# Kernel optimization log

Hardware: AMD Instinct MI355X
Metric: run time of the kernel (lower is better)

Reference implementation:

```python
import jax, jax.numpy as jnp
import numpy as np

N, E, E_LBL = 50000, 800000, 200000
D_IN, H = 128, 128


def setup_inputs() -> dict:
    key = jax.random.key(0)
    ks = jax.random.split(key, 12)
    s = 0.05
    return {
        "x": jax.random.normal(ks[0], (N, D_IN), jnp.float32),
        "edge_index": jax.random.randint(ks[1], (2, E), 0, N, jnp.int64),
        "edge_label_index": jax.random.randint(ks[2], (2, E_LBL), 0, N, jnp.int64),
        "pre_w": jax.random.normal(ks[3], (D_IN, H), jnp.float32) * s,
        "pre_b": jax.random.normal(ks[4], (H,), jnp.float32) * s,
        "Wx": jax.random.normal(ks[5], (3, 2, H, H), jnp.float32) * s,  # gates z,r,h x cheb orders T0,T1
        "bx": jax.random.normal(ks[6], (3, H), jnp.float32) * s,
        "Wh": jax.random.normal(ks[7], (3, 2, H, H), jnp.float32) * s,
        "bh": jax.random.normal(ks[8], (3, H), jnp.float32) * s,
        "post_w": jax.random.normal(ks[9], (H, 2), jnp.float32) * s,
        "post_b": jax.random.normal(ks[10], (2,), jnp.float32) * s,
    }


def reference(x, edge_index, edge_label_index, pre_w, pre_b, Wx, bx, Wh, bh, post_w, post_b):
    n = x.shape[0]
    src, dst = edge_index[0], edge_index[1]

    # Scaled Chebyshev Laplacian (sym norm, lambda_max=2): L_hat = -D^{-1/2} A D^{-1/2}
    # (diagonal of L_hat is exactly 0, so only off-diagonal edge terms remain).
    deg = jax.ops.segment_sum(jnp.ones_like(src, dtype=x.dtype), src, num_segments=n)
    dinv = jnp.where(deg > 0, jax.lax.rsqrt(jnp.maximum(deg, 1.0)), 0.0)
    w = -(dinv[src] * dinv[dst])  # [E]

    def lap(v):  # L_hat @ v : gather src rows, weight, scatter-add at dst
        return jax.ops.segment_sum(w[:, None] * v[src], dst, num_segments=n)

    def cheb(v, Lv, W2, b):  # ChebConv K=2: T0(v)@W0 + T1(v)@W1 + b
        return v @ W2[0] + Lv @ W2[1] + b

    # pre: Linear(input_dim -> hidden)
    Xh = x @ pre_w + pre_b  # [N, H]
    LX = lap(Xh)

    # GConvGRU single step, H0 = 0
    Hc = jnp.zeros_like(Xh)
    LH = lap(Hc)
    Z = jax.nn.sigmoid(cheb(Xh, LX, Wx[0], bx[0]) + cheb(Hc, LH, Wh[0], bh[0]))
    R = jax.nn.sigmoid(cheb(Xh, LX, Wx[1], bx[1]) + cheb(Hc, LH, Wh[1], bh[1]))
    HR = Hc * R
    LHR = lap(HR)
    Ht = jnp.tanh(cheb(Xh, LX, Wx[2], bx[2]) + cheb(HR, LHR, Wh[2], bh[2]))
    Hc = Z * Hc + (1.0 - Z) * Ht

    h = jax.nn.relu(Hc)
    # link decoder: gather endpoints, hadamard, Linear(H->2), sum over logits
    hprod = h[edge_label_index[0]] * h[edge_label_index[1]]  # [E_lbl, H]
    out = hprod @ post_w + post_b  # [E_lbl, 2]
    return jnp.sum(out, axis=-1)  # [E_lbl]
```

## Files before the change

kernel.cpp:

```cpp
#include <hip/hip_runtime.h>
#include <math.h>


#define RND 2048
#define SORT_CAP 1536
#define CAPB 6144

typedef __attribute__((ext_vector_type(4))) float f32x4;
typedef __attribute__((ext_vector_type(8))) short short8;
typedef __attribute__((ext_vector_type(4))) unsigned u32x4;
typedef __attribute__((ext_vector_type(4))) int i32x4;

static __device__ __forceinline__ unsigned short f2b(float f) {
  union { float f; unsigned u; } v; v.f = f;
  unsigned r = (v.u + 0x7fffu + ((v.u >> 16) & 1u)) >> 16;
  return (unsigned short)r;
}
static __device__ __forceinline__ float b2f(unsigned short s) {
  union { unsigned u; float f; } v; v.u = ((unsigned)s) << 16;
  return v.f;
}

__global__ __launch_bounds__(256) void prep_kernel(const float* __restrict__ pre_w, const float* __restrict__ Wx,
                                                   const float* __restrict__ bx, const float* __restrict__ bh,
                                                   const float* __restrict__ post_w, const float* __restrict__ post_b,
                                                   unsigned short* __restrict__ Bt1c, unsigned short* __restrict__ Btc2,
                                                   float* __restrict__ fb2, float* __restrict__ pwsum,
                                                   int* __restrict__ binPos) {
  int e = blockIdx.x * 256 + threadIdx.x;
  if (e < 512) binPos[e * 16] = (e & 255) * CAPB;
  if (e < 16384) {
    int kc = e >> 12, r = e & 4095, col = r >> 5, kk = r & 31;
    Bt1c[e] = f2b(pre_w[(kc * 32 + kk) * 128 + col]);
  }
  int e2 = e - 16384;
  if (e2 >= 0 && e2 < 65536) {
    int kc = e2 >> 13, r = e2 & 8191, cB = r >> 5, kk = r & 31;
    int k = kc * 32 + kk, half = k >> 7, ki = k & 127;
    int cb = cB >> 7, r7 = cB & 127, nw6 = r7 >> 6, u2 = r7 & 63;
    int g = (u2 >= 32) ? 2 : 0, hcol = cb * 64 + nw6 * 32 + (u2 & 31);
    Btc2[e2] = f2b(Wx[((g * 2 + half) * 128 + ki) * 128 + hcol]);
  }
  int e3 = e - (16384 + 65536);
  if (e3 >= 0 && e3 < 256) {
    int cB = e3;
    int cb = cB >> 7, r7 = cB & 127, nw6 = r7 >> 6, u2 = r7 & 63;
    int g = (u2 >= 32) ? 2 : 0, hcol = cb * 64 + nw6 * 32 + (u2 & 31);
    fb2[cB] = bx[g * 128 + hcol] + bh[g * 128 + hcol];
  }
  int e4 = e - (16384 + 65536 + 256);
  if (e4 >= 0 && e4 < 128) pwsum[e4] = post_w[2 * e4] + post_w[2 * e4 + 1];
  if (e4 == 128) pwsum[128] = post_b[0] + post_b[1];
}

union SMemU {
  struct { unsigned short As[128 * 40]; unsigned short Bs[128 * 40]; } g;
  struct { unsigned ent[RND]; int hist[256], lstart[256], lofs[256], gbase[256], wsum[4];
           unsigned char ebin[RND], sb[RND]; } s;
};

__global__ __launch_bounds__(256) void mega1_kernel(const float* __restrict__ x,
                                                    const unsigned short* __restrict__ Bt1c,
                                                    const float* __restrict__ pre_b,
                                                    unsigned short* __restrict__ Xq,
                                                    const int* __restrict__ ei, int* __restrict__ binPos,
                                                    unsigned* __restrict__ bins,
                                                    unsigned char* __restrict__ sbins,
                                                    int N, int E, int RB) {
  __shared__ SMemU sm;
  const int t = threadIdx.x;

  if ((int)blockIdx.x < RB) {
    unsigned short* As = sm.g.As;
    unsigned short* Bs = sm.g.Bs;
    const int r0 = blockIdx.x * 128;
    const int w = t >> 6, lane = t & 63;
    const int m = lane & 15, q = lane >> 4;
    const int mw = (w >> 1) * 64, nw = (w & 1) * 64;

    f32x4 acc[4][4];
#pragma unroll
    for (int i = 0; i < 4; ++i)
#pragma unroll
      for (int j = 0; j < 4; ++j) acc[i][j] = {0.f, 0.f, 0.f, 0.f};

    const int arow = t >> 1, aseg = t & 1;
    const bool arow_ok = (r0 + arow) < N;
    const float* asrc0 = &x[(size_t)(r0 + arow) * 128 + aseg * 16];

    float4 cav[4]; short8 cbv0, cbv1;
    {
      if (arow_ok) {
#pragma unroll
        for (int i = 0; i < 4; ++i) cav[i] = *(const float4*)(asrc0 + i * 4);
      } else {
#pragma unroll
        for (int i = 0; i < 4; ++i) cav[i] = make_float4(0.f, 0.f, 0.f, 0.f);
      }
      const char* src = (const char*)Bt1c + t * 32;
      cbv0 = *(const short8*)src;
      cbv1 = *(const short8*)(src + 16);
    }

    for (int kc = 0; kc < 4; ++kc) {
      __syncthreads();
      {
        short8 t0, t1;
#pragma unroll
        for (int i = 0; i < 2; ++i) {
          t0[i * 4 + 0] = (short)f2b(cav[i].x); t0[i * 4 + 1] = (short)f2b(cav[i].y);
          t0[i * 4 + 2] = (short)f2b(cav[i].z); t0[i * 4 + 3] = (short)f2b(cav[i].w);
          t1[i * 4 + 0] = (short)f2b(cav[i + 2].x); t1[i * 4 + 1] = (short)f2b(cav[i + 2].y);
          t1[i * 4 + 2] = (short)f2b(cav[i + 2].z); t1[i * 4 + 3] = (short)f2b(cav[i + 2].w);
        }
        *(short8*)&As[arow * 40 + aseg * 16] = t0;
        *(short8*)&As[arow * 40 + aseg * 16 + 8] = t1;
        int bcol = t >> 1, boff = (t & 1) * 16;
        *(short8*)&Bs[bcol * 40 + boff] = cbv0;
        *(short8*)&Bs[bcol * 40 + boff + 8] = cbv1;
      }
      float4 nav[4]; short8 nbv0, nbv1;
      if (kc < 3) {
        if (arow_ok) {
          const float* src = asrc0 + (kc + 1) * 32;
#pragma unroll
          for (int i = 0; i < 4; ++i) nav[i] = *(const float4*)(src + i * 4);
        } else {
#pragma unroll
          for (int i = 0; i < 4; ++i) nav[i] = make_float4(0.f, 0.f, 0.f, 0.f);
        }
        const char* src = (const char*)Bt1c + (size_t)(kc + 1) * 8192 + t * 32;
        nbv0 = *(const short8*)src;
        nbv1 = *(const short8*)(src + 16);
      }
      __syncthreads();
      short8 af[4], bf[4];
#pragma unroll
      for (int i = 0; i < 4; ++i) af[i] = *(const short8*)&As[(mw + i * 16 + m) * 40 + q * 8];
#pragma unroll
      for (int j = 0; j < 4; ++j) bf[j] = *(const short8*)&Bs[(nw + j * 16 + m) * 40 + q * 8];
#pragma unroll
      for (int i = 0; i < 4; ++i)
#pragma unroll
        for (int j = 0; j < 4; ++j)
          acc[i][j] = __builtin_amdgcn_mfma_f32_16x16x32_bf16(af[i], bf[j], acc[i][j], 0, 0, 0);
      if (kc < 3) {
#pragma unroll
        for (int i = 0; i < 4; ++i) cav[i] = nav[i];
        cbv0 = nbv0; cbv1 = nbv1;
      }
    }

#pragma unroll
    for (int i = 0; i < 4; ++i) {
      int rb2 = r0 + mw + i * 16 + q * 4;
#pragma unroll
      for (int j = 0; j < 4; ++j) {
        int col = nw + j * 16 + m;
        float bias = pre_b[col];
#pragma unroll
        for (int r = 0; r < 4; ++r) {
          int row = rb2 + r;
          if (row < N) Xq[(size_t)row * 128 + col] = f2b(acc[i][j][r] + bias);
        }
      }
    }
    return;
  }

  unsigned* ent = sm.s.ent;
  unsigned char* ebin = sm.s.ebin;
  unsigned char* sb = sm.s.sb;
  int* hist = sm.s.hist;
  int* lstart = sm.s.lstart;
  int* lofs = sm.s.lofs;
  int* gbase = sm.s.gbase;
  int* wsum = sm.s.wsum;
  const int sbid = (int)blockIdx.x - RB;
  const int snum = (int)gridDim.x - RB;
  const int w = t >> 6, lane = t & 63;
  for (long long base = (long long)sbid * RND; base < E; base += (long long)snum * RND) {
    int cnt = (int)(((long long)E - base < RND) ? (E - base) : RND);
    if (t < 256) hist[t] = 0;
    __syncthreads();
    int my_s[8], my_d[8];
    {
      long long e0 = base + (long long)t * 8;
      if (e0 + 8 <= E && 8 * t + 8 <= cnt) {
        const i32x4* ps = (const i32x4*)&ei[e0];
        const i32x4* pd = (const i32x4*)&ei[E + e0];
        i32x4 s0 = ps[0], s1 = ps[1], d0 = pd[0], d1 = pd[1];
#pragma unroll
        for (int u = 0; u < 4; ++u) { my_s[u] = s0[u]; my_d[u] = d0[u]; }
#pragma unroll
        for (int u = 0; u < 4; ++u) { my_s[4 + u] = s1[u]; my_d[4 + u] = d1[u]; }
      } else {
#pragma unroll
        for (int u = 0; u < 8; ++u) {
          int i = t * 8 + u;
          my_s[u] = -1;
          if (i < cnt) { my_s[u] = ei[base + i]; my_d[u] = ei[E + base + i]; }
        }
      }
#pragma unroll
      for (int u = 0; u < 8; ++u)
        if (my_s[u] >= 0) atomicAdd(&hist[my_d[u] >> 8], 1);
    }
    __syncthreads();
    {
      int h = hist[t];
      hist[t] = 0;
      int v = h;
#pragma unroll
      for (int dd = 1; dd < 64; dd <<= 1) { int uu = __shfl_up(v, dd); if (lane >= dd) v += uu; }
      if (lane == 63) wsum[w] = v;
      __syncthreads();
      int woff = 0;
#pragma unroll
      for (int ww = 0; ww < 3; ++ww) if (ww < w) woff += wsum[ww];
      int excl = v - h + woff;
      lstart[t] = excl; lofs[t] = excl;
      if (h > 0) gbase[t] = atomicAdd(&binPos[t * 16], h);
    }
    __syncthreads();
#pragma unroll
    for (int u = 0; u < 8; ++u) {
      if (my_s[u] >= 0) {
        int b = my_d[u] >> 8;
        int p = atomicAdd(&lofs[b], 1);
        ent[p] = (unsigned)my_s[u] | ((unsigned)(my_d[u] & 255) << 16) | ((unsigned)b << 24);
        atomicAdd(&hist[my_s[u] >> 8], 1);
      }
    }
    __syncthreads();
    for (int i = t; i < cnt; i += 256) {
      unsigned e = ent[i];
      int b = e >> 24;
      int pos = gbase[b] + (i - lstart[b]);
      if (pos < (b + 1) * CAPB) bins[pos] = e;
    }
    __syncthreads();
    {
      int h = hist[t];
      int v = h;
#pragma unroll
      for (int dd = 1; dd < 64; dd <<= 1) { int uu = __shfl_up(v, dd); if (lane >= dd) v += uu; }
      if (lane == 63) wsum[w] = v;
      __syncthreads();
      int woff = 0;
#pragma unroll
      for (int ww = 0; ww < 3; ++ww) if (ww < w) woff += wsum[ww];
      int excl = v - h + woff;
      lstart[t] = excl; lofs[t] = excl;
      if (h > 0) gbase[t] = atomicAdd(&binPos[(256 + t) * 16], h);
    }
    __syncthreads();
#pragma unroll
    for (int u = 0; u < 8; ++u) {
      if (my_s[u] >= 0) {
        int b = my_s[u] >> 8;
        int p = atomicAdd(&lofs[b], 1);
        sb[p] = (unsigned char)(my_s[u] & 255);
        ebin[p] = (unsigned char)b;
      }
    }
    __syncthreads();
    for (int i = t; i < cnt; i += 256) {
      int b = ebin[i];
      int pos = gbase[b] + (i - lstart[b]);
      if (pos < (b + 1) * CAPB) sbins[pos] = sb[i];
    }
    __syncthreads();
  }
}

__global__ __launch_bounds__(256) void deghist_kernel(const unsigned char* __restrict__ sbins,
                                                      const int* __restrict__ binPos,
                                                      float* __restrict__ dinv, int N) {
  __shared__ int h[256];
  const int t = threadIdx.x;
  const int bin = blockIdx.x;
  h[t] = 0;
  __syncthreads();
  int T2 = binPos[(256 + bin) * 16] - bin * CAPB;
  if (T2 > CAPB) T2 = CAPB;
  const unsigned char* __restrict__ p = sbins + (size_t)bin * CAPB;
  for (int i = t; i < T2; i += 256) atomicAdd(&h[p[i]], 1);
  __syncthreads();
  int node = bin * 256 + t;
  if (node < N) dinv[node] = h[t] > 0 ? rsqrtf((float)h[t]) : 0.0f;
}

__global__ __launch_bounds__(512) void lap_bin_kernel(const unsigned short* __restrict__ Xq,
                                                      unsigned short* __restrict__ LXc,
                                                      const unsigned* __restrict__ bins,
                                                      const int* __restrict__ binPos,
                                                      const float* __restrict__ dinv, int N) {
  __shared__ unsigned eLDS[CAPB];
  __shared__ unsigned short sortS[SORT_CAP];
  __shared__ float sortW[SORT_CAP];
  __shared__ int hist[64], start[64], off[64];
  const int t = threadIdx.x;
  const int bin = blockIdx.x >> 2, qt = blockIdx.x & 3;
  const int lo = bin * CAPB;
  int T = binPos[bin * 16] - lo;
  if (T > CAPB) T = CAPB;
  const unsigned* __restrict__ ebase = &bins[lo];
  if (t < 64) hist[t] = 0;
  __syncthreads();
  for (int i = t; i < T; i += 512) {
    unsigned e = ebase[i];
    eLDS[i] = e;
    int dl = (e >> 16) & 255;
    if ((dl >> 6) == qt) atomicAdd(&hist[dl & 63], 1);
  }
  __syncthreads();
  if (t < 64) {
    int h = hist[t];
    int v = h;
#pragma unroll
    for (int d = 1; d < 64; d <<= 1) {
      int u = __shfl_up(v, d);
      if (t >= d) v += u;
    }
    start[t] = v - h;
    off[t] = v - h;
  }
  __syncthreads();
  for (int i = t; i < T; i += 512) {
    unsigned e = eLDS[i];
    int dl = (e >> 16) & 255;
    if ((dl >> 6) == qt) {
      int p = atomicAdd(&off[dl & 63], 1);
      if (p < SORT_CAP) {
        int s = (int)(e & 0xFFFFu);
        sortS[p] = (unsigned short)s;
        sortW[p] = dinv[s];
      }
    }
  }
  __syncthreads();
  const int wv = t >> 6, lane = t & 63;
  const int g4 = lane >> 4, sl = lane & 15;
  for (int n = wv; n < 64; n += 8) {
    int node = bin * 256 + qt * 64 + n;
    if (node >= N) break;
    int st = start[n], cnum = hist[n];
    float acc[8] = {0.f, 0.f, 0.f, 0.f, 0.f, 0.f, 0.f, 0.f};
    for (int j = 0; j < cnum; j += 8) {
#pragma unroll
      for (int u = 0; u < 2; ++u) {
        int idx = j + u * 4 + g4;
        bool val = idx < cnum;
        int si = st + (val ? idx : 0);
        int s = sortS[si];
        float ws = sortW[si];
        u32x4 vv = *(const u32x4*)((const char*)Xq + (size_t)s * 256 + sl * 16);
        if (val) {
#pragma unroll
          for (int k = 0; k < 4; ++k) {
            union { unsigned u32; float f; } fl, fh;
            fl.u32 = vv[k] << 16; fh.u32 = vv[k] & 0xffff0000u;
            acc[2 * k] += ws * fl.f;
            acc[2 * k + 1] += ws * fh.f;
          }
        }
      }
    }
#pragma unroll
    for (int k = 0; k < 8; ++k) {
      acc[k] += __shfl_xor(acc[k], 16);
      acc[k] += __shfl_xor(acc[k], 32);
    }
    if (g4 == 0) {
      float wd = -dinv[node];
      u32x4 o;
#pragma unroll
      for (int k = 0; k < 4; ++k)
        o[k] = (unsigned)f2b(acc[2 * k] * wd) | ((unsigned)f2b(acc[2 * k + 1] * wd) << 16);
      *(u32x4*)((char*)LXc + (size_t)node * 256 + sl * 16) = o;
    }
  }
}

__global__ __launch_bounds__(256) void gemm2_mfma(const unsigned short* __restrict__ Xq,
                                                  const unsigned short* __restrict__ LXc,
                                                  const unsigned short* __restrict__ Btc2,
                                                  const float* __restrict__ fb2,
                                                  unsigned short* __restrict__ hb, int N) {
  const int t = threadIdx.x;
  const int rb = blockIdx.x >> 1, cb = blockIdx.x & 1;
  const int r0 = rb * 128;
  const int w = t >> 6, lane = t & 63;
  const int m = lane & 15, q = lane >> 4;
  const int mw = (w >> 1) * 64, nw = (w & 1) * 64;

  f32x4 acc[4][4];
#pragma unroll
  for (int i = 0; i < 4; ++i)
#pragma unroll
    for (int j = 0; j < 4; ++j) acc[i][j] = {0.f, 0.f, 0.f, 0.f};

  size_t aoff[4];
#pragma unroll
  for (int i = 0; i < 4; ++i)
    aoff[i] = (size_t)(r0 + mw + i * 16 + m) * 256 + (size_t)q * 16;
  const char* bbase = (const char*)Btc2 + (size_t)(cb * 128 + nw + m) * 64 + (size_t)q * 16;

#pragma unroll 2
  for (int kc = 0; kc < 8; ++kc) {
    const char* abase = (kc < 4) ? (const char*)Xq : (const char*)LXc;
    const size_t ko = (size_t)(kc & 3) * 64;
    short8 af[4], bf[4];
#pragma unroll
    for (int i = 0; i < 4; ++i)
      af[i] = *(const short8*)(abase + aoff[i] + ko);
    const char* bk = bbase + (size_t)kc * 16384;
#pragma unroll
    for (int j = 0; j < 4; ++j)
      bf[j] = *(const short8*)(bk + (size_t)j * 16 * 64);
#pragma unroll
    for (int i = 0; i < 4; ++i)
#pragma unroll
      for (int j = 0; j < 4; ++j)
        acc[i][j] = __builtin_amdgcn_mfma_f32_16x16x32_bf16(af[i], bf[j], acc[i][j], 0, 0, 0);
  }

#pragma unroll
  for (int i = 0; i < 4; ++i) {
    int rbase = r0 + mw + i * 16 + q * 4;
#pragma unroll
    for (int jz = 0; jz < 2; ++jz) {
      int cBz = cb * 128 + nw + jz * 16 + m;
      int hc = cb * 64 + (nw >> 1) + jz * 16 + m;
      float bz = fb2[cBz], bt = fb2[cBz + 32];
#pragma unroll
      for (int r = 0; r < 4; ++r) {
        int row = rbase + r;
        if (row < N) {
          float zp = acc[i][jz][r] + bz;
          float tp = acc[i][jz + 2][r] + bt;
          float zs = 1.0f / (1.0f + __expf(-zp));
          float th = tanhf(tp);
          hb[(size_t)row * 128 + hc] = f2b(fmaxf((1.0f - zs) * th, 0.0f));
        }
      }
    }
  }
}

__global__ __launch_bounds__(256) void decoder_kernel(const unsigned short* __restrict__ hb,
                                                      const int* __restrict__ eli,
                                                      const float* __restrict__ pwsum, float* __restrict__ out, int M) {
  int t = threadIdx.x;
  int i = blockIdx.x * 16 + (t >> 4);
  int l = t & 15;
  if (i >= M) return;
  int a = eli[i], b = eli[M + i];
  int k = l * 8;
  short8 va = *(const short8*)&hb[(size_t)a * 128 + k];
  short8 vb = *(const short8*)&hb[(size_t)b * 128 + k];
  const float4* pwp = (const float4*)&pwsum[k];
  float4 p0 = pwp[0], p1 = pwp[1];
  float s = 0.0f;
  s += b2f((unsigned short)va[0]) * b2f((unsigned short)vb[0]) * p0.x;
  s += b2f((unsigned short)va[1]) * b2f((unsigned short)vb[1]) * p0.y;
  s += b2f((unsigned short)va[2]) * b2f((unsigned short)vb[2]) * p0.z;
  s += b2f((unsigned short)va[3]) * b2f((unsigned short)vb[3]) * p0.w;
  s += b2f((unsigned short)va[4]) * b2f((unsigned short)vb[4]) * p1.x;
  s += b2f((unsigned short)va[5]) * b2f((unsigned short)vb[5]) * p1.y;
  s += b2f((unsigned short)va[6]) * b2f((unsigned short)vb[6]) * p1.z;
  s += b2f((unsigned short)va[7]) * b2f((unsigned short)vb[7]) * p1.w;
#pragma unroll
  for (int off = 8; off; off >>= 1) s += __shfl_xor(s, off);
  if (l == 0) out[i] = s + pwsum[128];
}

extern "C" void kernel_launch(void* const* d_in, const int* in_sizes, int n_in,
                              void* d_out, int out_size, void* d_ws, size_t ws_size,
                              hipStream_t stream) {
  const float* x      = (const float*)d_in[0];
  const int*   ei     = (const int*)d_in[1];
  const int*   eli    = (const int*)d_in[2];
  const float* pre_w  = (const float*)d_in[3];
  const float* pre_b  = (const float*)d_in[4];
  const float* Wx     = (const float*)d_in[5];
  const float* bx     = (const float*)d_in[6];
  const float* bh     = (const float*)d_in[8];
  const float* post_w = (const float*)d_in[9];
  const float* post_b = (const float*)d_in[10];
  float* out = (float*)d_out;

  const int N = in_sizes[0] / 128;
  const int E = in_sizes[1] / 2;
  const int M = in_sizes[2] / 2;
  const int RB = (N + 127) / 128;
  const int NBIN = (N + 255) / 256;
  const int SCAT = (E + RND - 1) / RND;

  char* W = (char*)d_ws;
  size_t o = 0;
  float* dinv = (float*)(W + o); o += (size_t)N * 4;
  o = (o + 255) & ~(size_t)255;
  int* binPos = (int*)(W + o);    o += 512 * 16 * 4;
  o = (o + 255) & ~(size_t)255;
  unsigned* bins = (unsigned*)(W + o); o += (size_t)NBIN * CAPB * 4;
  o = (o + 255) & ~(size_t)255;
  unsigned char* sbins = (unsigned char*)(W + o); o += (size_t)NBIN * CAPB;
  o = (o + 255) & ~(size_t)255;
  unsigned short* Xq = (unsigned short*)(W + o);  o += (size_t)RB * 128 * 256;
  unsigned short* LXc = (unsigned short*)(W + o); o += (size_t)RB * 128 * 256;
  unsigned short* hb = (unsigned short*)(W + o);  o += (size_t)N * 256;
  unsigned short* Bt1c = (unsigned short*)(W + o); o += 32768;
  unsigned short* Btc2 = (unsigned short*)(W + o); o += 131072;
  float* fb2 = (float*)(W + o);  o += 1024;
  float* pwsum = (float*)(W + o); o += 768;

  prep_kernel<<<322, 256, 0, stream>>>(pre_w, Wx, bx, bh, post_w, post_b, Bt1c, Btc2, fb2, pwsum,
                                       binPos);
  mega1_kernel<<<RB + SCAT, 256, 0, stream>>>(x, Bt1c, pre_b, Xq, ei, binPos, bins, sbins, N, E, RB);
  deghist_kernel<<<NBIN, 256, 0, stream>>>(sbins, binPos, dinv, N);
  lap_bin_kernel<<<NBIN * 4, 512, 0, stream>>>(Xq, LXc, bins, binPos, dinv, N);
  gemm2_mfma<<<RB * 2, 256, 0, stream>>>(Xq, LXc, Btc2, fb2, hb, N);
  decoder_kernel<<<(M + 15) / 16, 256, 0, stream>>>(hb, eli, pwsum, out, M);
}
```

Baseline: 210.1 us.

## Split gemm2 across 8 waves and double-buffer fragment loads

The gemm2 MFMA kernel now runs 512 threads per block, giving each wave half the output columns (a z/tanh column pair) so per-wave accumulators shrink from 16 to 8 tiles. The k-loop is fully unrolled with ping-pong register buffers, so the next k-chunk's A/B fragments load while the current chunk's MFMAs run. The intent is to hide global load latency and raise occupancy through lower register pressure. The cost is that every A fragment is now loaded by twice as many waves.

```diff
diff --git a/kernel.cpp b/kernel.cpp
--- a/kernel.cpp
+++ b/kernel.cpp
@@ -383,7 +383,7 @@
   }
 }
 
-__global__ __launch_bounds__(256) void gemm2_mfma(const unsigned short* __restrict__ Xq,
+__global__ __launch_bounds__(512) void gemm2_mfma(const unsigned short* __restrict__ Xq,
                                                   const unsigned short* __restrict__ LXc,
                                                   const unsigned short* __restrict__ Btc2,
                                                   const float* __restrict__ fb2,
@@ -393,57 +393,78 @@
   const int r0 = rb * 128;
   const int w = t >> 6, lane = t & 63;
   const int m = lane & 15, q = lane >> 4;
-  const int mw = (w >> 1) * 64, nw = (w & 1) * 64;
-
-  f32x4 acc[4][4];
-#pragma unroll
-  for (int i = 0; i < 4; ++i)
-#pragma unroll
-    for (int j = 0; j < 4; ++j) acc[i][j] = {0.f, 0.f, 0.f, 0.f};
+  const int mw = (w >> 2) * 64;
+  const int wc = w & 3;
+  const int nw64 = (wc >> 1) * 64, jo = wc & 1;
+  const int cZ = cb * 128 + nw64 + jo * 16 + m;
+
+  f32x4 acc[4][2];
+#pragma unroll
+  for (int i = 0; i < 4; ++i) { acc[i][0] = {0.f,0.f,0.f,0.f}; acc[i][1] = {0.f,0.f,0.f,0.f}; }
 
   size_t aoff[4];
 #pragma unroll
   for (int i = 0; i < 4; ++i)
     aoff[i] = (size_t)(r0 + mw + i * 16 + m) * 256 + (size_t)q * 16;
-  const char* bbase = (const char*)Btc2 + (size_t)(cb * 128 + nw + m) * 64 + (size_t)q * 16;
-
-#pragma unroll 2
+  const char* bbase = (const char*)Btc2 + (size_t)cZ * 64 + (size_t)q * 16;
+
+  short8 afA[4], bfA[2], afB[4], bfB[2];
+  {
+    const char* ab = (const char*)Xq;
+#pragma unroll
+    for (int i = 0; i < 4; ++i) afA[i] = *(const short8*)(ab + aoff[i]);
+    bfA[0] = *(const short8*)(bbase);
+    bfA[1] = *(const short8*)(bbase + 32 * 64);
+  }
+#pragma unroll
   for (int kc = 0; kc < 8; ++kc) {
-    const char* abase = (kc < 4) ? (const char*)Xq : (const char*)LXc;
-    const size_t ko = (size_t)(kc & 3) * 64;
-    short8 af[4], bf[4];
-#pragma unroll
-    for (int i = 0; i < 4; ++i)
-      af[i] = *(const short8*)(abase + aoff[i] + ko);
-    const char* bk = bbase + (size_t)kc * 16384;
-#pragma unroll
-    for (int j = 0; j < 4; ++j)
-      bf[j] = *(const short8*)(bk + (size_t)j * 16 * 64);
-#pragma unroll
-    for (int i = 0; i < 4; ++i)
-#pragma unroll
-      for (int j = 0; j < 4; ++j)
-        acc[i][j] = __builtin_amdgcn_mfma_f32_16x16x32_bf16(af[i], bf[j], acc[i][j], 0, 0, 0);
-  }
-
+    const bool even = (kc & 1) == 0;
+    if (kc < 7) {
+      const int kn = kc + 1;
+      const char* ab = (kn < 4) ? (const char*)Xq : (const char*)LXc;
+      const size_t ko = (size_t)(kn & 3) * 64;
+      const char* bk = bbase + (size_t)kn * 16384;
+      if (even) {
+#pragma unroll
+        for (int i = 0; i < 4; ++i) afB[i] = *(const short8*)(ab + aoff[i] + ko);
+        bfB[0] = *(const short8*)(bk);
+        bfB[1] = *(const short8*)(bk + 32 * 64);
+      } else {
+#pragma unroll
+        for (int i = 0; i < 4; ++i) afA[i] = *(const short8*)(ab + aoff[i] + ko);
+        bfA[0] = *(const short8*)(bk);
+        bfA[1] = *(const short8*)(bk + 32 * 64);
+      }
+    }
+    if (even) {
+#pragma unroll
+      for (int i = 0; i < 4; ++i) {
+        acc[i][0] = __builtin_amdgcn_mfma_f32_16x16x32_bf16(afA[i], bfA[0], acc[i][0], 0, 0, 0);
+        acc[i][1] = __builtin_amdgcn_mfma_f32_16x16x32_bf16(afA[i], bfA[1], acc[i][1], 0, 0, 0);
+      }
+    } else {
+#pragma unroll
+      for (int i = 0; i < 4; ++i) {
+        acc[i][0] = __builtin_amdgcn_mfma_f32_16x16x32_bf16(afB[i], bfB[0], acc[i][0], 0, 0, 0);
+        acc[i][1] = __builtin_amdgcn_mfma_f32_16x16x32_bf16(afB[i], bfB[1], acc[i][1], 0, 0, 0);
+      }
+    }
+  }
+
+  const float bz = fb2[cZ], bt = fb2[cZ + 32];
+  const int hc = cb * 64 + (nw64 >> 1) + jo * 16 + m;
 #pragma unroll
   for (int i = 0; i < 4; ++i) {
     int rbase = r0 + mw + i * 16 + q * 4;
 #pragma unroll
-    for (int jz = 0; jz < 2; ++jz) {
-      int cBz = cb * 128 + nw + jz * 16 + m;
-      int hc = cb * 64 + (nw >> 1) + jz * 16 + m;
-      float bz = fb2[cBz], bt = fb2[cBz + 32];
-#pragma unroll
-      for (int r = 0; r < 4; ++r) {
-        int row = rbase + r;
-        if (row < N) {
-          float zp = acc[i][jz][r] + bz;
-          float tp = acc[i][jz + 2][r] + bt;
-          float zs = 1.0f / (1.0f + __expf(-zp));
-          float th = tanhf(tp);
-          hb[(size_t)row * 128 + hc] = f2b(fmaxf((1.0f - zs) * th, 0.0f));
-        }
+    for (int r = 0; r < 4; ++r) {
+      int row = rbase + r;
+      if (row < N) {
+        float zp = acc[i][0][r] + bz;
+        float tp = acc[i][1][r] + bt;
+        float zs = 1.0f / (1.0f + __expf(-zp));
+        float th = tanhf(tp);
+        hb[(size_t)row * 128 + hc] = f2b(fmaxf((1.0f - zs) * th, 0.0f));
       }
     }
   }
@@ -521,6 +542,6 @@
   mega1_kernel<<<RB + SCAT, 256, 0, stream>>>(x, Bt1c, pre_b, Xq, ei, binPos, bins, sbins, N, E, RB);
   deghist_kernel<<<NBIN, 256, 0, stream>>>(sbins, binPos, dinv, N);
   lap_bin_kernel<<<NBIN * 4, 512, 0, stream>>>(Xq, LXc, bins, binPos, dinv, N);
-  gemm2_mfma<<<RB * 2, 256, 0, stream>>>(Xq, LXc, Btc2, fb2, hb, N);
+  gemm2_mfma<<<RB * 2, 512, 0, stream>>>(Xq, LXc, Btc2, fb2, hb, N);
   decoder_kernel<<<(M + 15) / 16, 256, 0, stream>>>(hb, eli, pwsum, out, M);
 }
```

Measured after the change: 216.6 us. +3.1%, slower.

## Fuse Laplacian aggregation with gate GEMM, keep LX tile in LDS

Applied to the files above, without the earlier changes.

Merges the binned Laplacian kernel and the MFMA gate GEMM into one kernel. Each 64-node block writes its bf16 L·X rows into LDS (reusing the edge staging buffer through a union) and then runs the second GEMM directly, reading Xq from global and LX from LDS. This removes the LX round trip through global memory and one kernel launch. In exchange each block computes a 64x256 output tile with 8 waves, which gives less B-matrix reuse than the old 128-row tiles, and the GEMM now waits behind the gather phase in every block.

```diff
diff --git a/kernel.cpp b/kernel.cpp
--- a/kernel.cpp
+++ b/kernel.cpp
@@ -291,12 +291,17 @@
   if (node < N) dinv[node] = h[t] > 0 ? rsqrtf((float)h[t]) : 0.0f;
 }
 
-__global__ __launch_bounds__(512) void lap_bin_kernel(const unsigned short* __restrict__ Xq,
-                                                      unsigned short* __restrict__ LXc,
-                                                      const unsigned* __restrict__ bins,
-                                                      const int* __restrict__ binPos,
-                                                      const float* __restrict__ dinv, int N) {
-  __shared__ unsigned eLDS[CAPB];
+__global__ __launch_bounds__(512) void lap_gemm2_kernel(const unsigned short* __restrict__ Xq,
+                                                        const unsigned* __restrict__ bins,
+                                                        const int* __restrict__ binPos,
+                                                        const float* __restrict__ dinv,
+                                                        const unsigned short* __restrict__ Btc2,
+                                                        const float* __restrict__ fb2,
+                                                        unsigned short* __restrict__ hb, int N) {
+  __shared__ union {
+    unsigned eLDS[CAPB];
+    unsigned short lx[64 * 136];
+  } u;
   __shared__ unsigned short sortS[SORT_CAP];
   __shared__ float sortW[SORT_CAP];
   __shared__ int hist[64], start[64], off[64];
@@ -310,7 +315,7 @@
   __syncthreads();
   for (int i = t; i < T; i += 512) {
     unsigned e = ebase[i];
-    eLDS[i] = e;
+    u.eLDS[i] = e;
     int dl = (e >> 16) & 255;
     if ((dl >> 6) == qt) atomicAdd(&hist[dl & 63], 1);
   }
@@ -320,15 +325,15 @@
     int v = h;
 #pragma unroll
     for (int d = 1; d < 64; d <<= 1) {
-      int u = __shfl_up(v, d);
-      if (t >= d) v += u;
+      int uu = __shfl_up(v, d);
+      if (t >= d) v += uu;
     }
     start[t] = v - h;
     off[t] = v - h;
   }
   __syncthreads();
   for (int i = t; i < T; i += 512) {
-    unsigned e = eLDS[i];
+    unsigned e = u.eLDS[i];
     int dl = (e >> 16) & 255;
     if ((dl >> 6) == qt) {
       int p = atomicAdd(&off[dl & 63], 1);
@@ -349,8 +354,8 @@
     float acc[8] = {0.f, 0.f, 0.f, 0.f, 0.f, 0.f, 0.f, 0.f};
     for (int j = 0; j < cnum; j += 8) {
 #pragma unroll
-      for (int u = 0; u < 2; ++u) {
-        int idx = j + u * 4 + g4;
+      for (int uu = 0; uu < 2; ++uu) {
+        int idx = j + uu * 4 + g4;
         bool val = idx < cnum;
         int si = st + (val ? idx : 0);
         int s = sortS[si];
@@ -378,57 +383,58 @@
 #pragma unroll
       for (int k = 0; k < 4; ++k)
         o[k] = (unsigned)f2b(acc[2 * k] * wd) | ((unsigned)f2b(acc[2 * k + 1] * wd) << 16);
-      *(u32x4*)((char*)LXc + (size_t)node * 256 + sl * 16) = o;
-    }
-  }
-}
-
-__global__ __launch_bounds__(256) void gemm2_mfma(const unsigned short* __restrict__ Xq,
-                                                  const unsigned short* __restrict__ LXc,
-                                                  const unsigned short* __restrict__ Btc2,
-                                                  const float* __restrict__ fb2,
-                                                  unsigned short* __restrict__ hb, int N) {
-  const int t = threadIdx.x;
-  const int rb = blockIdx.x >> 1, cb = blockIdx.x & 1;
-  const int r0 = rb * 128;
-  const int w = t >> 6, lane = t & 63;
+      *(u32x4*)((char*)u.lx + (size_t)n * 272 + sl * 16) = o;
+    }
+  }
+  __syncthreads();
+
   const int m = lane & 15, q = lane >> 4;
-  const int mw = (w >> 1) * 64, nw = (w & 1) * 64;
-
-  f32x4 acc[4][4];
-#pragma unroll
-  for (int i = 0; i < 4; ++i)
-#pragma unroll
-    for (int j = 0; j < 4; ++j) acc[i][j] = {0.f, 0.f, 0.f, 0.f};
-
-  size_t aoff[4];
-#pragma unroll
-  for (int i = 0; i < 4; ++i)
-    aoff[i] = (size_t)(r0 + mw + i * 16 + m) * 256 + (size_t)q * 16;
+  const int mwl = (wv >> 2) * 32;
+  const int wc = wv & 3;
+  const int cb = wc >> 1, nw = (wc & 1) * 64;
+  const int r0 = bin * 256 + qt * 64;
+
+  f32x4 acc2[2][4];
+#pragma unroll
+  for (int i = 0; i < 2; ++i)
+#pragma unroll
+    for (int j = 0; j < 4; ++j) acc2[i][j] = {0.f, 0.f, 0.f, 0.f};
+
+  size_t aoff[2];
+#pragma unroll
+  for (int i = 0; i < 2; ++i) {
+    int ar = r0 + mwl + i * 16 + m;
+    if (ar >= N) ar = 0;
+    aoff[i] = (size_t)ar * 256 + (size_t)q * 16;
+  }
   const char* bbase = (const char*)Btc2 + (size_t)(cb * 128 + nw + m) * 64 + (size_t)q * 16;
 
-#pragma unroll 2
+#pragma unroll
   for (int kc = 0; kc < 8; ++kc) {
-    const char* abase = (kc < 4) ? (const char*)Xq : (const char*)LXc;
-    const size_t ko = (size_t)(kc & 3) * 64;
-    short8 af[4], bf[4];
-#pragma unroll
-    for (int i = 0; i < 4; ++i)
-      af[i] = *(const short8*)(abase + aoff[i] + ko);
+    short8 af[2], bf[4];
+    if (kc < 4) {
+#pragma unroll
+      for (int i = 0; i < 2; ++i)
+        af[i] = *(const short8*)((const char*)Xq + aoff[i] + (size_t)kc * 64);
+    } else {
+#pragma unroll
+      for (int i = 0; i < 2; ++i)
+        af[i] = *(const short8*)((const char*)u.lx + (size_t)(mwl + i * 16 + m) * 272 + (size_t)q * 16 + (size_t)(kc - 4) * 64);
+    }
     const char* bk = bbase + (size_t)kc * 16384;
 #pragma unroll
     for (int j = 0; j < 4; ++j)
-      bf[j] = *(const short8*)(bk + (size_t)j * 16 * 64);
-#pragma unroll
-    for (int i = 0; i < 4; ++i)
+      bf[j] = *(const short8*)(bk + (size_t)j * 1024);
+#pragma unroll
+    for (int i = 0; i < 2; ++i)
 #pragma unroll
       for (int j = 0; j < 4; ++j)
-        acc[i][j] = __builtin_amdgcn_mfma_f32_16x16x32_bf16(af[i], bf[j], acc[i][j], 0, 0, 0);
-  }
-
-#pragma unroll
-  for (int i = 0; i < 4; ++i) {
-    int rbase = r0 + mw + i * 16 + q * 4;
+        acc2[i][j] = __builtin_amdgcn_mfma_f32_16x16x32_bf16(af[i], bf[j], acc2[i][j], 0, 0, 0);
+  }
+
+#pragma unroll
+  for (int i = 0; i < 2; ++i) {
+    int rbase = r0 + mwl + i * 16 + q * 4;
 #pragma unroll
     for (int jz = 0; jz < 2; ++jz) {
       int cBz = cb * 128 + nw + jz * 16 + m;
@@ -438,8 +444,8 @@
       for (int r = 0; r < 4; ++r) {
         int row = rbase + r;
         if (row < N) {
-          float zp = acc[i][jz][r] + bz;
-          float tp = acc[i][jz + 2][r] + bt;
+          float zp = acc2[i][jz][r] + bz;
+          float tp = acc2[i][jz + 2][r] + bt;
           float zs = 1.0f / (1.0f + __expf(-zp));
           float th = tanhf(tp);
           hb[(size_t)row * 128 + hc] = f2b(fmaxf((1.0f - zs) * th, 0.0f));
@@ -509,7 +515,6 @@
   unsigned char* sbins = (unsigned char*)(W + o); o += (size_t)NBIN * CAPB;
   o = (o + 255) & ~(size_t)255;
   unsigned short* Xq = (unsigned short*)(W + o);  o += (size_t)RB * 128 * 256;
-  unsigned short* LXc = (unsigned short*)(W + o); o += (size_t)RB * 128 * 256;
   unsigned short* hb = (unsigned short*)(W + o);  o += (size_t)N * 256;
   unsigned short* Bt1c = (unsigned short*)(W + o); o += 32768;
   unsigned short* Btc2 = (unsigned short*)(W + o); o += 131072;
@@ -520,7 +525,6 @@
                                        binPos);
   mega1_kernel<<<RB + SCAT, 256, 0, stream>>>(x, Bt1c, pre_b, Xq, ei, binPos, bins, sbins, N, E, RB);
   deghist_kernel<<<NBIN, 256, 0, stream>>>(sbins, binPos, dinv, N);
-  lap_bin_kernel<<<NBIN * 4, 512, 0, stream>>>(Xq, LXc, bins, binPos, dinv, N);
-  gemm2_mfma<<<RB * 2, 256, 0, stream>>>(Xq, LXc, Btc2, fb2, hb, N);
+  lap_gemm2_kernel<<<NBIN * 4, 512, 0, stream>>>(Xq, bins, binPos, dinv, Btc2, fb2, hb, N);
   decoder_kernel<<<(M + 15) / 16, 256, 0, stream>>>(hb, eli, pwsum, out, M);
 }
```

Result: slower. 219.7 us (+4.5%).
